# Kernel tuning notes

Measured on AMD Instinct MI355X. Metric: run time of the kernel, lower is better.

## Reference

```python
import jax, jax.numpy as jnp
import numpy as np

B, L, E, H, W = 2, 8192, 1024, 16, 128
HD = E // H  # 64


def setup_inputs() -> dict:
    key = jax.random.key(0)
    ks = jax.random.split(key, 9)
    s = 1.0 / np.sqrt(E)
    inp = {"x": jax.random.normal(ks[0], (B, L, E), jnp.float32)}
    for i, n in enumerate(["Wq", "Wk", "Wv", "Wo"]):
        inp[n] = jax.random.uniform(ks[1 + i], (E, E), jnp.float32, -s, s)
    for i, n in enumerate(["bq", "bk", "bv", "bo"]):
        inp[n] = jax.random.uniform(ks[5 + i], (E,), jnp.float32, -s, s)
    return inp


def _skew_prob(p, w):
    # (..., w, 2w+1) -> (..., w, 3w) with row i right-shifted by i:
    # out[..., i, i+j] = p[..., i, j]  (zeros elsewhere)
    lead = p.shape[:-2]
    M, Lc = p.shape[-2], p.shape[-1]
    p = jnp.pad(p, [(0, 0)] * len(lead) + [(0, 0), (0, M + 1)])
    p = p.reshape(*lead, M * (Lc + M + 1))[..., :-M].reshape(*lead, M, M + Lc)
    return p[..., :-1]


def _sliding_attend(q, k, v, w):
    # q,k,v: (b,h,l,d); banded attention, window w on each side (2w+1 diagonals)
    b, h, l, d = q.shape
    c = l // w
    qc = q.reshape(b, h, c, w, d)
    # per-chunk key/value windows of 3w tokens (w halo each side, zero padded)
    idx = jnp.arange(c)[:, None] * w + jnp.arange(3 * w)[None, :]  # (c, 3w)
    kw = jnp.pad(k, ((0, 0), (0, 0), (w, w), (0, 0)))[:, :, idx]  # (b,h,c,3w,d)
    s = jnp.einsum('bhcqd,bhckd->bhcqk', qc, kw)  # (b,h,c,w,3w)
    # extract band: band[i, j] = s[i, i+j], j in [0, 2w] (offset d = j - w)
    gidx = (jnp.arange(w)[:, None] + jnp.arange(2 * w + 1)[None, :])[None, None, None]
    band = jnp.take_along_axis(s, gidx, axis=-1).reshape(b, h, l, 2 * w + 1)
    # mask out-of-range positions (matches the module's edge -inf loop)
    pos = jnp.arange(l)[:, None] + (jnp.arange(2 * w + 1) - w)[None, :]
    band = jnp.where((pos >= 0) & (pos < l), band, -jnp.inf)
    prob = jax.nn.softmax(band / np.sqrt(d), axis=-1)  # scale by sqrt(head_dim)
    vw = jnp.pad(v, ((0, 0), (0, 0), (w, w), (0, 0)))[:, :, idx]  # (b,h,c,3w,d)
    p3 = _skew_prob(prob.reshape(b, h, c, w, 2 * w + 1), w)  # (b,h,c,w,3w)
    ctx = jnp.einsum('bhcqk,bhckd->bhcqd', p3, vw)
    return ctx.reshape(b, h, l, d)


def reference(x, Wq, Wk, Wv, Wo, bq, bk, bv, bo):
    q = (x @ Wq.T + bq).reshape(B, L, H, HD).transpose(0, 2, 1, 3)
    k = (x @ Wk.T + bk).reshape(B, L, H, HD).transpose(0, 2, 1, 3)
    v = (x @ Wv.T + bv).reshape(B, L, H, HD).transpose(0, 2, 1, 3)
    ctx = _sliding_attend(q, k, v, W)
    ctx = ctx.transpose(0, 2, 1, 3).reshape(B, L, E)
    return ctx @ Wo.T + bo
```

## Files before the change

### kernel.cpp

```cpp
#include <hip/hip_runtime.h>
#include <math.h>

#define B_SZ  2
#define L_SEQ 8192
#define EMB   1024
#define NH    16
#define HDIM  64
#define WIN   128
#define MROWS (B_SZ*L_SEQ)

typedef __attribute__((ext_vector_type(8))) _Float16 f16x8;
typedef __attribute__((ext_vector_type(4))) _Float16 f16x4;
typedef __attribute__((ext_vector_type(4))) float f32x4;

__device__ __forceinline__ void gload16(const void* g, void* l) {
    __builtin_amdgcn_global_load_lds(
        (const __attribute__((address_space(1))) unsigned int*)g,
        (__attribute__((address_space(3))) unsigned int*)l, 16, 0, 0);
}

__global__ __launch_bounds__(256)
void round_all(const float* __restrict__ x,
               const float* __restrict__ wq, const float* __restrict__ wk,
               const float* __restrict__ wv, const float* __restrict__ wo,
               _Float16* __restrict__ xf, _Float16* __restrict__ q16,
               _Float16* __restrict__ k16, _Float16* __restrict__ v16,
               _Float16* __restrict__ o16)
{
    const size_t NX = (size_t)MROWS * EMB, NW = (size_t)EMB * EMB;
    size_t gid = ((size_t)blockIdx.x * 256 + threadIdx.x) * 4;
    const float* src; _Float16* dst; size_t off;
    if (gid < NX)               { src = x;  dst = xf;  off = gid; }
    else if (gid < NX + NW)     { src = wq; dst = q16; off = gid - NX; }
    else if (gid < NX + 2*NW)   { src = wk; dst = k16; off = gid - NX - 2*NW + NW; }
    else if (gid < NX + 3*NW)   { src = wv; dst = v16; off = gid - NX - 2*NW; }
    else                        { src = wo; dst = o16; off = gid - NX - 3*NW; }
    float4 v = *(const float4*)(src + off);
    f16x4 o;
    o[0] = (_Float16)v.x; o[1] = (_Float16)v.y;
    o[2] = (_Float16)v.z; o[3] = (_Float16)v.w;
    *(f16x4*)(dst + off) = o;
}

__global__ __launch_bounds__(256)
void gemm_qkv(const _Float16* __restrict__ X,
              const _Float16* __restrict__ Wq, const _Float16* __restrict__ Wk,
              const _Float16* __restrict__ Wv,
              const float* __restrict__ bq, const float* __restrict__ bk,
              const float* __restrict__ bv,
              _Float16* __restrict__ qf, _Float16* __restrict__ kf,
              _Float16* __restrict__ vtf)
{
    constexpr int K = EMB;
    __shared__ char smem[34816];
    _Float16* As = (_Float16*)smem;
    _Float16* Bs = (_Float16*)(smem + 16384);

    const int id = blockIdx.x;
    const int row = (id / 192) * 8 + (id & 7);
    const int colq = (id >> 3) % 24;
    const int wsel = colq >> 3;
    const int bm = row * 128, bn = (colq & 7) * 128;
    const _Float16* Bw = wsel == 0 ? Wq : wsel == 1 ? Wk : Wv;
    const float* bias = wsel == 0 ? bq : wsel == 1 ? bk : bv;
    const float scale = wsel == 0 ? 0.125f : 1.0f;

    const int t = threadIdx.x;
    const int wave = t >> 6, lane = t & 63;
    const int srow = t >> 3;
    const int gq8 = ((t & 7) ^ (srow & 7)) * 8;
    size_t gA[4], gB[4];
    #pragma unroll
    for (int s = 0; s < 4; s++) {
        int r = s * 32 + srow;
        gA[s] = (size_t)(bm + r) * K + gq8;
        gB[s] = (size_t)(bn + r) * K + gq8;
    }
    const int lbw = wave * 1024;

    const int wr = wave >> 1, wc = wave & 1;
    const int frow = lane & 15, quad = lane >> 4;
    int aoff[4][2], boff[4][2];
    #pragma unroll
    for (int i = 0; i < 4; i++)
        #pragma unroll
        for (int ks = 0; ks < 2; ks++) {
            int slot = ((ks * 4 + quad) ^ (frow & 7)) * 16;
            aoff[i][ks] = (wr * 64 + i * 16 + frow) * 128 + slot;
            boff[i][ks] = (wc * 64 + i * 16 + frow) * 128 + slot;
        }

    f32x4 acc[4][4] = {};
    for (int k0 = 0; k0 < K; k0 += 64) {
        #pragma unroll
        for (int s = 0; s < 4; s++) {
            gload16(X  + gA[s] + k0, (char*)As + s * 4096 + lbw);
            gload16(Bw + gB[s] + k0, (char*)Bs + s * 4096 + lbw);
        }
        __syncthreads();
        #pragma unroll
        for (int ks = 0; ks < 2; ks++) {
            f16x8 af[4], bf[4];
            #pragma unroll
            for (int i = 0; i < 4; i++) {
                af[i] = *(const f16x8*)((const char*)As + aoff[i][ks]);
                bf[i] = *(const f16x8*)((const char*)Bs + boff[i][ks]);
            }
            #pragma unroll
            for (int i = 0; i < 4; i++)
                #pragma unroll
                for (int j = 0; j < 4; j++)
                    acc[i][j] = __builtin_amdgcn_mfma_f32_16x16x32_f16(af[i], bf[j], acc[i][j], 0, 0, 0);
        }
        __syncthreads();
    }

    _Float16* Ct = (_Float16*)smem;
    const int ccol = lane & 15;
    if (wsel < 2) {
        #pragma unroll
        for (int i = 0; i < 4; i++)
            #pragma unroll
            for (int j = 0; j < 4; j++) {
                int nl = wc * 64 + j * 16 + ccol;
                float bvv = bias[bn + nl];
                #pragma unroll
                for (int r = 0; r < 4; r++) {
                    int ml = wr * 64 + i * 16 + quad * 4 + r;
                    Ct[ml * 136 + nl] = (_Float16)((acc[i][j][r] + bvv) * scale);
                }
            }
        __syncthreads();
        _Float16* dst = wsel == 0 ? qf : kf;
        #pragma unroll
        for (int pass = 0; pass < 8; pass++) {
            int chunk = pass * 256 + t;
            int ml = chunk >> 4, seg = chunk & 15;
            uint4 v = *(const uint4*)&Ct[ml * 136 + seg * 8];
            int m = bm + ml, bb = m >> 13, l = m & (L_SEQ - 1);
            int n = bn + seg * 8, h = n >> 6, d = n & 63;
            *(uint4*)&dst[((size_t)(bb * NH + h) * L_SEQ + l) * HDIM + d] = v;
        }
    } else {
        #pragma unroll
        for (int i = 0; i < 4; i++)
            #pragma unroll
            for (int j = 0; j < 4; j++) {
                int nl = wc * 64 + j * 16 + ccol;
                float bvv = bias[bn + nl];
                #pragma unroll
                for (int r = 0; r < 4; r++) {
                    int ml = wr * 64 + i * 16 + quad * 4 + r;
                    Ct[nl * 136 + ml] = (_Float16)(acc[i][j][r] + bvv);
                }
            }
        __syncthreads();
        #pragma unroll
        for (int pass = 0; pass < 8; pass++) {
            int chunk = pass * 256 + t;
            int nl = chunk >> 4, seg = chunk & 15;
            uint4 v = *(const uint4*)&Ct[nl * 136 + seg * 8];
            int n = bn + nl, h = n >> 6, d = n & 63;
            int bb = bm >> 13, l = (bm & (L_SEQ - 1)) + seg * 8;
            *(uint4*)&vtf[((size_t)(bb * NH + h) * HDIM + d) * L_SEQ + l] = v;
        }
    }
}

__global__ __launch_bounds__(256)
void gemm_out(const _Float16* __restrict__ A, const _Float16* __restrict__ Bw,
              const float* __restrict__ bias, float* __restrict__ C)
{
    constexpr int K = EMB, N = EMB;
    __shared__ char smem[32768];
    _Float16* As = (_Float16*)smem;
    _Float16* Bs = (_Float16*)(smem + 16384);

    const int id = blockIdx.x;
    const int row = (id / 64) * 8 + (id & 7);
    const int bm = row * 128, bn = ((id >> 3) & 7) * 128;

    const int t = threadIdx.x;
    const int wave = t >> 6, lane = t & 63;
    const int srow = t >> 3;
    const int gq8 = ((t & 7) ^ (srow & 7)) * 8;
    size_t gA[4], gB[4];
    #pragma unroll
    for (int s = 0; s < 4; s++) {
        int r = s * 32 + srow;
        gA[s] = (size_t)(bm + r) * K + gq8;
        gB[s] = (size_t)(bn + r) * K + gq8;
    }
    const int lbw = wave * 1024;

    const int wr = wave >> 1, wc = wave & 1;
    const int frow = lane & 15, quad = lane >> 4;
    int aoff[4][2], boff[4][2];
    #pragma unroll
    for (int i = 0; i < 4; i++)
        #pragma unroll
        for (int ks = 0; ks < 2; ks++) {
            int slot = ((ks * 4 + quad) ^ (frow & 7)) * 16;
            aoff[i][ks] = (wr * 64 + i * 16 + frow) * 128 + slot;
            boff[i][ks] = (wc * 64 + i * 16 + frow) * 128 + slot;
        }

    f32x4 acc[4][4] = {};
    for (int k0 = 0; k0 < K; k0 += 64) {
        #pragma unroll
        for (int s = 0; s < 4; s++) {
            gload16(A  + gA[s] + k0, (char*)As + s * 4096 + lbw);
            gload16(Bw + gB[s] + k0, (char*)Bs + s * 4096 + lbw);
        }
        __syncthreads();
        #pragma unroll
        for (int ks = 0; ks < 2; ks++) {
            f16x8 af[4], bf[4];
            #pragma unroll
            for (int i = 0; i < 4; i++) {
                af[i] = *(const f16x8*)((const char*)As + aoff[i][ks]);
                bf[i] = *(const f16x8*)((const char*)Bs + boff[i][ks]);
            }
            #pragma unroll
            for (int i = 0; i < 4; i++)
                #pragma unroll
                for (int j = 0; j < 4; j++)
                    acc[i][j] = __builtin_amdgcn_mfma_f32_16x16x32_f16(af[i], bf[j], acc[i][j], 0, 0, 0);
        }
        __syncthreads();
    }

    const int ccol = lane & 15;
    #pragma unroll
    for (int i = 0; i < 4; i++) {
        int m0 = bm + wr * 64 + i * 16 + quad * 4;
        #pragma unroll
        for (int j = 0; j < 4; j++) {
            int n = bn + wc * 64 + j * 16 + ccol;
            float bvv = bias[n];
            #pragma unroll
            for (int r = 0; r < 4; r++)
                C[(size_t)(m0 + r) * N + n] = acc[i][j][r] + bvv;
        }
    }
}

__global__ __launch_bounds__(256)
void attn_mfma(const _Float16* __restrict__ qf, const _Float16* __restrict__ kf,
               const _Float16* __restrict__ vtf, _Float16* __restrict__ cf)
{
    __shared__ _Float16 Kf[4096], Vf[4096];
    __shared__ _Float16 Ps[4][16 * 72];

    const int t = threadIdx.x;
    const int wave = t >> 6, lane = t & 63;
    const int col = lane & 15, quad = lane >> 4;
    const int bh = blockIdx.y;
    const int q0 = blockIdx.x * 128;

    f16x8 qfr[2][2];
    #pragma unroll
    for (int g = 0; g < 2; g++) {
        size_t qidx = ((size_t)bh * L_SEQ + q0 + g * 64 + wave * 16 + col) * HDIM + quad * 8;
        qfr[g][0] = *(const f16x8*)(qf + qidx);
        qfr[g][1] = *(const f16x8*)(qf + qidx + 32);
    }

    f32x4 o[2][4] = {};
    float mrun[2][4], lrun[2][4];
    #pragma unroll
    for (int g = 0; g < 2; g++)
        #pragma unroll
        for (int r = 0; r < 4; r++) { mrun[g][r] = -3e38f; lrun[g][r] = 0.0f; }

    const int srow = t >> 3, sc = t & 7;
    _Float16* Pw = Ps[wave];

    for (int kt = 0; kt < 6; kt++) {
        const int p0 = q0 - WIN + kt * 64;
        if (p0 < 0 || p0 >= L_SEQ) continue;
        #pragma unroll
        for (int sw = 0; sw < 2; sw++) {
            int row = sw * 32 + srow;
            int gq = sc ^ (row & 7);
            size_t kgi = ((size_t)bh * L_SEQ + p0 + row) * HDIM + gq * 8;
            size_t vgi = ((size_t)bh * HDIM + row) * L_SEQ + p0 + gq * 8;
            int lb = sw * 4096 + wave * 1024;
            gload16(kf + kgi, (char*)Kf + lb);
            gload16(vtf + vgi, (char*)Vf + lb);
        }
        __syncthreads();

        #pragma unroll
        for (int g = 0; g < 2; g++) {
            f32x4 s[4] = {};
            #pragma unroll
            for (int ks = 0; ks < 2; ks++)
                #pragma unroll
                for (int n = 0; n < 4; n++) {
                    int off = (n * 16 + col) * 128 + (((ks * 4 + quad) ^ (col & 7)) * 16);
                    f16x8 kfr = *(const f16x8*)((const char*)Kf + off);
                    s[n] = __builtin_amdgcn_mfma_f32_16x16x32_f16(qfr[g][ks], kfr, s[n], 0, 0, 0);
                }
            const int rowb = q0 + g * 64 + wave * 16 + quad * 4;
            #pragma unroll
            for (int n = 0; n < 4; n++)
                #pragma unroll
                for (int r = 0; r < 4; r++) {
                    int dlt = (p0 + n * 16 + col) - (rowb + r);
                    if (dlt < -WIN || dlt > WIN) s[n][r] = -3e38f;
                }
            float mx[4];
            #pragma unroll
            for (int r = 0; r < 4; r++)
                mx[r] = fmaxf(fmaxf(s[0][r], s[1][r]), fmaxf(s[2][r], s[3][r]));
            #pragma unroll
            for (int x = 1; x < 16; x <<= 1)
                #pragma unroll
                for (int r = 0; r < 4; r++)
                    mx[r] = fmaxf(mx[r], __shfl_xor(mx[r], x, 64));
            float alpha[4];
            #pragma unroll
            for (int r = 0; r < 4; r++) {
                float mn = fmaxf(mrun[g][r], mx[r]);
                alpha[r] = __expf(mrun[g][r] - mn);
                mrun[g][r] = mn;
            }
            float sm[4] = {0.f, 0.f, 0.f, 0.f};
            #pragma unroll
            for (int n = 0; n < 4; n++)
                #pragma unroll
                for (int r = 0; r < 4; r++) {
                    float pv = __expf(s[n][r] - mrun[g][r]);
                    sm[r] += pv;
                    Pw[(quad * 4 + r) * 72 + n * 16 + col] = (_Float16)pv;
                }
            #pragma unroll
            for (int x = 1; x < 16; x <<= 1)
                #pragma unroll
                for (int r = 0; r < 4; r++)
                    sm[r] += __shfl_xor(sm[r], x, 64);
            #pragma unroll
            for (int r = 0; r < 4; r++)
                lrun[g][r] = lrun[g][r] * alpha[r] + sm[r];
            #pragma unroll
            for (int n = 0; n < 4; n++)
                #pragma unroll
                for (int r = 0; r < 4; r++)
                    o[g][n][r] *= alpha[r];
            #pragma unroll
            for (int ks = 0; ks < 2; ks++) {
                f16x8 pfr = *(const f16x8*)&Pw[col * 72 + ks * 32 + quad * 8];
                #pragma unroll
                for (int n = 0; n < 4; n++) {
                    int off = (n * 16 + col) * 128 + (((ks * 4 + quad) ^ (col & 7)) * 16);
                    f16x8 vfr = *(const f16x8*)((const char*)Vf + off);
                    o[g][n] = __builtin_amdgcn_mfma_f32_16x16x32_f16(pfr, vfr, o[g][n], 0, 0, 0);
                }
            }
        }
        __syncthreads();
    }

    const int b = bh >> 4, h = bh & 15;
    #pragma unroll
    for (int g = 0; g < 2; g++)
        #pragma unroll
        for (int r = 0; r < 4; r++) {
            float inv = 1.0f / lrun[g][r];
            int q = q0 + g * 64 + wave * 16 + quad * 4 + r;
            size_t base = ((size_t)b * L_SEQ + q) * EMB + h * HDIM;
            #pragma unroll
            for (int n = 0; n < 4; n++)
                cf[base + n * 16 + col] = (_Float16)(o[g][n][r] * inv);
        }
}

extern "C" void kernel_launch(void* const* d_in, const int* in_sizes, int n_in,
                              void* d_out, int out_size, void* d_ws, size_t ws_size,
                              hipStream_t stream) {
    const float* x  = (const float*)d_in[0];
    const float* Wq = (const float*)d_in[1];
    const float* Wk = (const float*)d_in[2];
    const float* Wv = (const float*)d_in[3];
    const float* Wo = (const float*)d_in[4];
    const float* bq = (const float*)d_in[5];
    const float* bk = (const float*)d_in[6];
    const float* bv = (const float*)d_in[7];
    const float* bo = (const float*)d_in[8];
    float* out = (float*)d_out;

    const size_t per = (size_t)B_SZ * NH * L_SEQ * HDIM;
    _Float16* w16 = (_Float16*)d_ws;
    _Float16* xf   = w16;
    _Float16* qf   = w16 + per;
    _Float16* kf   = w16 + 2 * per;
    _Float16* vtf  = w16 + 3 * per;
    _Float16* cf   = w16 + 4 * per;
    _Float16* wq16 = w16 + 5 * per;
    _Float16* wk16 = wq16 + 1048576;
    _Float16* wv16 = wq16 + 2 * 1048576;
    _Float16* wo16 = wq16 + 3 * 1048576;

    dim3 blk(256);
    const int nround = (MROWS * EMB + 4 * EMB * EMB) / 1024;
    round_all<<<nround, blk, 0, stream>>>(x, Wq, Wk, Wv, Wo, xf, wq16, wk16, wv16, wo16);

    gemm_qkv<<<3072, blk, 0, stream>>>(xf, wq16, wk16, wv16, bq, bk, bv, qf, kf, vtf);

    attn_mfma<<<dim3(L_SEQ / 128, B_SZ * NH), blk, 0, stream>>>(qf, kf, vtf, cf);

    gemm_out<<<1024, blk, 0, stream>>>(cf, wo16, bo, out);
}
```

Measured before the change: 386.4 us.

## Use 256x256 double-buffered 512-thread tiles for QKV and output GEMMs

Both projection GEMMs move from 128x128 tiles with 256 threads to 256x256 tiles with 512 threads (8 waves, each computing 128x64) and a K step of 32. A two-stage LDS ring is filled by global_load_lds, with explicit vmcnt waits and barriers so the next tile's loads overlap the current MFMAs, and s_setprio is raised around the MFMA bursts. The QKV epilogue now stages through per-wave swizzled LDS before the coalesced stores to q, k and transposed v. This aims for more data reuse per loaded byte and better latency hiding, at the cost of 64KB of LDS per block, more registers and fewer blocks in the grid.

Result: no change. 381.4 us (-1.3%).

```diff
diff --git a/kernel.cpp b/kernel.cpp
--- a/kernel.cpp
+++ b/kernel.cpp
@@ -42,7 +42,82 @@
     *(f16x4*)(dst + off) = o;
 }
 
-__global__ __launch_bounds__(256)
+
+#define QKV_LOOP_PROLOGUE(Aptr, Bptr)                                          \
+    const int t = threadIdx.x;                                                 \
+    const int wave = t >> 6, lane = t & 63;                                    \
+    const int wr = wave >> 2, wc = wave & 3;                                   \
+    const int frow = lane & 15, quad = lane >> 4;                              \
+    const int srow = t >> 2;                                                   \
+    const int schunk = (t & 3) ^ ((t >> 3) & 3);                               \
+    size_t gA[2], gB[2];                                                       \
+    _Pragma("unroll")                                                          \
+    for (int s = 0; s < 2; ++s) {                                              \
+        int r = s * 128 + srow;                                                \
+        gA[s] = (size_t)(bm + r) * 1024 + schunk * 8;                          \
+        gB[s] = (size_t)(bn + r) * 1024 + schunk * 8;                          \
+    }                                                                          \
+    const int ldst = t * 16;                                                   \
+    const int sw = (quad ^ ((frow >> 1) & 3)) * 16;                            \
+    int aoff[8], boff[4];                                                      \
+    _Pragma("unroll")                                                          \
+    for (int i = 0; i < 8; ++i) aoff[i] = (wr * 128 + i * 16 + frow) * 64 + sw;\
+    _Pragma("unroll")                                                          \
+    for (int j = 0; j < 4; ++j)                                                \
+        boff[j] = 32768 + (wc * 64 + j * 16 + frow) * 64 + sw;                 \
+    f32x4 acc[8][4] = {};                                                      \
+    _Pragma("unroll")                                                          \
+    for (int pt = 0; pt < 2; ++pt)                                             \
+        _Pragma("unroll")                                                      \
+        for (int s = 0; s < 2; ++s) {                                          \
+            gload16(Aptr + gA[s] + pt * 32, smem + pt * 16384 + s * 8192 + ldst);          \
+            gload16(Bptr + gB[s] + pt * 32, smem + 32768 + pt * 16384 + s * 8192 + ldst);  \
+        }                                                                      \
+    for (int kt = 0; kt < 32; ++kt) {                                          \
+        const int cur = kt & 1;                                                \
+        if (kt < 31) asm volatile("s_waitcnt vmcnt(4)");                       \
+        else         asm volatile("s_waitcnt vmcnt(0)");                       \
+        __builtin_amdgcn_s_barrier();                                          \
+        asm volatile("" ::: "memory");                                         \
+        const char* Ab = (const char*)smem + cur * 16384;                      \
+        f16x8 af[4], bf[4];                                                    \
+        _Pragma("unroll")                                                      \
+        for (int j = 0; j < 4; ++j) bf[j] = *(const f16x8*)(Ab + boff[j] * 2 - boff[j] + boff[j]); \
+        _Pragma("unroll")                                                      \
+        for (int j = 0; j < 4; ++j) bf[j] = *(const f16x8*)(Ab + boff[j]);     \
+        _Pragma("unroll")                                                      \
+        for (int i = 0; i < 4; ++i) af[i] = *(const f16x8*)(Ab + aoff[i] * 1); \
+        __builtin_amdgcn_s_setprio(1);                                         \
+        _Pragma("unroll")                                                      \
+        for (int i = 0; i < 4; ++i)                                            \
+            _Pragma("unroll")                                                  \
+            for (int j = 0; j < 4; ++j)                                        \
+                acc[i][j] = __builtin_amdgcn_mfma_f32_16x16x32_f16(af[i], bf[j], acc[i][j], 0, 0, 0); \
+        __builtin_amdgcn_s_setprio(0);                                         \
+        _Pragma("unroll")                                                      \
+        for (int i = 0; i < 4; ++i) af[i] = *(const f16x8*)(Ab + aoff[i + 4]); \
+        __builtin_amdgcn_s_setprio(1);                                         \
+        _Pragma("unroll")                                                      \
+        for (int i = 0; i < 4; ++i)                                            \
+            _Pragma("unroll")                                                  \
+            for (int j = 0; j < 4; ++j)                                        \
+                acc[i + 4][j] = __builtin_amdgcn_mfma_f32_16x16x32_f16(af[i], bf[j], acc[i + 4][j], 0, 0, 0); \
+        __builtin_amdgcn_s_setprio(0);                                         \
+        asm volatile("" ::: "memory");                                         \
+        __builtin_amdgcn_s_barrier();                                          \
+        asm volatile("" ::: "memory");                                         \
+        if (kt + 2 < 32) {                                                     \
+            const int ko = (kt + 2) * 32;                                      \
+            _Pragma("unroll")                                                  \
+            for (int s = 0; s < 2; ++s) {                                      \
+                gload16(Aptr + gA[s] + ko, smem + cur * 16384 + s * 8192 + ldst);          \
+                gload16(Bptr + gB[s] + ko, smem + 32768 + cur * 16384 + s * 8192 + ldst);  \
+            }                                                                  \
+        }                                                                      \
+    }
+
+
+__global__ __launch_bounds__(512, 2)
 void gemm_qkv(const _Float16* __restrict__ X,
               const _Float16* __restrict__ Wq, const _Float16* __restrict__ Wk,
               const _Float16* __restrict__ Wv,
@@ -51,195 +126,105 @@
               _Float16* __restrict__ qf, _Float16* __restrict__ kf,
               _Float16* __restrict__ vtf)
 {
-    constexpr int K = EMB;
-    __shared__ char smem[34816];
-    _Float16* As = (_Float16*)smem;
-    _Float16* Bs = (_Float16*)(smem + 16384);
+    __shared__ __attribute__((aligned(16))) char smem[65536];
 
     const int id = blockIdx.x;
-    const int row = (id / 192) * 8 + (id & 7);
-    const int colq = (id >> 3) % 24;
-    const int wsel = colq >> 3;
-    const int bm = row * 128, bn = (colq & 7) * 128;
+    const int row = (id / 96) * 8 + (id & 7);
+    const int colq = (id >> 3) % 12;
+    const int wsel = colq >> 2;
+    const int bm = row * 256, bn = (colq & 3) * 256;
     const _Float16* Bw = wsel == 0 ? Wq : wsel == 1 ? Wk : Wv;
     const float* bias = wsel == 0 ? bq : wsel == 1 ? bk : bv;
     const float scale = wsel == 0 ? 0.125f : 1.0f;
 
-    const int t = threadIdx.x;
-    const int wave = t >> 6, lane = t & 63;
-    const int srow = t >> 3;
-    const int gq8 = ((t & 7) ^ (srow & 7)) * 8;
-    size_t gA[4], gB[4];
-    #pragma unroll
-    for (int s = 0; s < 4; s++) {
-        int r = s * 32 + srow;
-        gA[s] = (size_t)(bm + r) * K + gq8;
-        gB[s] = (size_t)(bn + r) * K + gq8;
-    }
-    const int lbw = wave * 1024;
-
-    const int wr = wave >> 1, wc = wave & 1;
-    const int frow = lane & 15, quad = lane >> 4;
-    int aoff[4][2], boff[4][2];
-    #pragma unroll
-    for (int i = 0; i < 4; i++)
-        #pragma unroll
-        for (int ks = 0; ks < 2; ks++) {
-            int slot = ((ks * 4 + quad) ^ (frow & 7)) * 16;
-            aoff[i][ks] = (wr * 64 + i * 16 + frow) * 128 + slot;
-            boff[i][ks] = (wc * 64 + i * 16 + frow) * 128 + slot;
-        }
-
-    f32x4 acc[4][4] = {};
-    for (int k0 = 0; k0 < K; k0 += 64) {
-        #pragma unroll
-        for (int s = 0; s < 4; s++) {
-            gload16(X  + gA[s] + k0, (char*)As + s * 4096 + lbw);
-            gload16(Bw + gB[s] + k0, (char*)Bs + s * 4096 + lbw);
-        }
-        __syncthreads();
-        #pragma unroll
-        for (int ks = 0; ks < 2; ks++) {
-            f16x8 af[4], bf[4];
-            #pragma unroll
-            for (int i = 0; i < 4; i++) {
-                af[i] = *(const f16x8*)((const char*)As + aoff[i][ks]);
-                bf[i] = *(const f16x8*)((const char*)Bs + boff[i][ks]);
+    QKV_LOOP_PROLOGUE(X, Bw)
+
+    char* Cw = smem + wave * 8192;
+    const int bb = bm >> 13;
+    const int l0 = (bm & (L_SEQ - 1)) + wr * 128;
+    const int h = (bn >> 6) + wc;
+    if (wsel < 2) {
+        _Float16* dst = wsel == 0 ? qf : kf;
+        const size_t hb = ((size_t)(bb * NH + h)) * L_SEQ * HDIM;
+        #pragma unroll
+        for (int ih = 0; ih < 2; ++ih) {
+            asm volatile("" ::: "memory");
+            #pragma unroll
+            for (int i = 0; i < 4; ++i)
+                #pragma unroll
+                for (int j = 0; j < 4; ++j) {
+                    const int lc = j * 16 + frow;
+                    const float bvv = bias[bn + wc * 64 + lc];
+                    #pragma unroll
+                    for (int r = 0; r < 4; ++r) {
+                        const int lr = i * 16 + quad * 4 + r;
+                        const int bo = lr * 128 + ((lc * 2) ^ ((lr & 7) << 4));
+                        *(_Float16*)(Cw + bo) = (_Float16)((acc[ih * 4 + i][j][r] + bvv) * scale);
+                    }
+                }
+            asm volatile("" ::: "memory");
+            #pragma unroll
+            for (int p = 0; p < 8; ++p) {
+                const int idx = p * 64 + lane;
+                const int lr = idx >> 3, seg = idx & 7;
+                const int bo = lr * 128 + ((seg * 16) ^ ((lr & 7) << 4));
+                uint4 v = *(const uint4*)(Cw + bo);
+                *(uint4*)&dst[hb + (size_t)(l0 + ih * 64 + lr) * HDIM + seg * 8] = v;
             }
-            #pragma unroll
-            for (int i = 0; i < 4; i++)
-                #pragma unroll
-                for (int j = 0; j < 4; j++)
-                    acc[i][j] = __builtin_amdgcn_mfma_f32_16x16x32_f16(af[i], bf[j], acc[i][j], 0, 0, 0);
-        }
-        __syncthreads();
-    }
-
-    _Float16* Ct = (_Float16*)smem;
-    const int ccol = lane & 15;
-    if (wsel < 2) {
-        #pragma unroll
-        for (int i = 0; i < 4; i++)
-            #pragma unroll
-            for (int j = 0; j < 4; j++) {
-                int nl = wc * 64 + j * 16 + ccol;
-                float bvv = bias[bn + nl];
-                #pragma unroll
-                for (int r = 0; r < 4; r++) {
-                    int ml = wr * 64 + i * 16 + quad * 4 + r;
-                    Ct[ml * 136 + nl] = (_Float16)((acc[i][j][r] + bvv) * scale);
-                }
+        }
+    } else {
+        const size_t hb = ((size_t)(bb * NH + h)) * HDIM * L_SEQ;
+        #pragma unroll
+        for (int ih = 0; ih < 2; ++ih) {
+            asm volatile("" ::: "memory");
+            #pragma unroll
+            for (int i = 0; i < 4; ++i)
+                #pragma unroll
+                for (int j = 0; j < 4; ++j) {
+                    const int lc = j * 16 + frow;
+                    const float bvv = bias[bn + wc * 64 + lc];
+                    #pragma unroll
+                    for (int r = 0; r < 4; ++r) {
+                        const int lr = i * 16 + quad * 4 + r;
+                        const int bo = lc * 128 + ((lr * 2) ^ ((lc & 7) << 4));
+                        *(_Float16*)(Cw + bo) = (_Float16)(acc[ih * 4 + i][j][r] + bvv);
+                    }
+                }
+            asm volatile("" ::: "memory");
+            #pragma unroll
+            for (int p = 0; p < 8; ++p) {
+                const int idx = p * 64 + lane;
+                const int dc = idx >> 3, sl = idx & 7;
+                const int bo = dc * 128 + ((sl * 16) ^ ((dc & 7) << 4));
+                uint4 v = *(const uint4*)(Cw + bo);
+                *(uint4*)&vtf[hb + (size_t)dc * L_SEQ + (l0 + ih * 64 + sl * 8)] = v;
             }
-        __syncthreads();
-        _Float16* dst = wsel == 0 ? qf : kf;
-        #pragma unroll
-        for (int pass = 0; pass < 8; pass++) {
-            int chunk = pass * 256 + t;
-            int ml = chunk >> 4, seg = chunk & 15;
-            uint4 v = *(const uint4*)&Ct[ml * 136 + seg * 8];
-            int m = bm + ml, bb = m >> 13, l = m & (L_SEQ - 1);
-            int n = bn + seg * 8, h = n >> 6, d = n & 63;
-            *(uint4*)&dst[((size_t)(bb * NH + h) * L_SEQ + l) * HDIM + d] = v;
-        }
-    } else {
-        #pragma unroll
-        for (int i = 0; i < 4; i++)
-            #pragma unroll
-            for (int j = 0; j < 4; j++) {
-                int nl = wc * 64 + j * 16 + ccol;
-                float bvv = bias[bn + nl];
-                #pragma unroll
-                for (int r = 0; r < 4; r++) {
-                    int ml = wr * 64 + i * 16 + quad * 4 + r;
-                    Ct[nl * 136 + ml] = (_Float16)(acc[i][j][r] + bvv);
-                }
-            }
-        __syncthreads();
-        #pragma unroll
-        for (int pass = 0; pass < 8; pass++) {
-            int chunk = pass * 256 + t;
-            int nl = chunk >> 4, seg = chunk & 15;
-            uint4 v = *(const uint4*)&Ct[nl * 136 + seg * 8];
-            int n = bn + nl, h = n >> 6, d = n & 63;
-            int bb = bm >> 13, l = (bm & (L_SEQ - 1)) + seg * 8;
-            *(uint4*)&vtf[((size_t)(bb * NH + h) * HDIM + d) * L_SEQ + l] = v;
-        }
-    }
-}
-
-__global__ __launch_bounds__(256)
-void gemm_out(const _Float16* __restrict__ A, const _Float16* __restrict__ Bw,
+        }
+    }
+}
+
+__global__ __launch_bounds__(512, 2)
+void gemm_out(const _Float16* __restrict__ A, const _Float16* __restrict__ Bwm,
               const float* __restrict__ bias, float* __restrict__ C)
 {
-    constexpr int K = EMB, N = EMB;
-    __shared__ char smem[32768];
-    _Float16* As = (_Float16*)smem;
-    _Float16* Bs = (_Float16*)(smem + 16384);
+    constexpr int N = EMB;
+    __shared__ __attribute__((aligned(16))) char smem[65536];
 
     const int id = blockIdx.x;
-    const int row = (id / 64) * 8 + (id & 7);
-    const int bm = row * 128, bn = ((id >> 3) & 7) * 128;
-
-    const int t = threadIdx.x;
-    const int wave = t >> 6, lane = t & 63;
-    const int srow = t >> 3;
-    const int gq8 = ((t & 7) ^ (srow & 7)) * 8;
-    size_t gA[4], gB[4];
+    const int row = (id / 32) * 8 + (id & 7);
+    const int bm = row * 256, bn = ((id >> 3) & 3) * 256;
+
+    QKV_LOOP_PROLOGUE(A, Bwm)
+
     #pragma unroll
-    for (int s = 0; s < 4; s++) {
-        int r = s * 32 + srow;
-        gA[s] = (size_t)(bm + r) * K + gq8;
-        gB[s] = (size_t)(bn + r) * K + gq8;
-    }
-    const int lbw = wave * 1024;
-
-    const int wr = wave >> 1, wc = wave & 1;
-    const int frow = lane & 15, quad = lane >> 4;
-    int aoff[4][2], boff[4][2];
-    #pragma unroll
-    for (int i = 0; i < 4; i++)
-        #pragma unroll
-        for (int ks = 0; ks < 2; ks++) {
-            int slot = ((ks * 4 + quad) ^ (frow & 7)) * 16;
-            aoff[i][ks] = (wr * 64 + i * 16 + frow) * 128 + slot;
-            boff[i][ks] = (wc * 64 + i * 16 + frow) * 128 + slot;
-        }
-
-    f32x4 acc[4][4] = {};
-    for (int k0 = 0; k0 < K; k0 += 64) {
-        #pragma unroll
-        for (int s = 0; s < 4; s++) {
-            gload16(A  + gA[s] + k0, (char*)As + s * 4096 + lbw);
-            gload16(Bw + gB[s] + k0, (char*)Bs + s * 4096 + lbw);
-        }
-        __syncthreads();
-        #pragma unroll
-        for (int ks = 0; ks < 2; ks++) {
-            f16x8 af[4], bf[4];
-            #pragma unroll
-            for (int i = 0; i < 4; i++) {
-                af[i] = *(const f16x8*)((const char*)As + aoff[i][ks]);
-                bf[i] = *(const f16x8*)((const char*)Bs + boff[i][ks]);
-            }
-            #pragma unroll
-            for (int i = 0; i < 4; i++)
-                #pragma unroll
-                for (int j = 0; j < 4; j++)
-                    acc[i][j] = __builtin_amdgcn_mfma_f32_16x16x32_f16(af[i], bf[j], acc[i][j], 0, 0, 0);
-        }
-        __syncthreads();
-    }
-
-    const int ccol = lane & 15;
-    #pragma unroll
-    for (int i = 0; i < 4; i++) {
-        int m0 = bm + wr * 64 + i * 16 + quad * 4;
-        #pragma unroll
-        for (int j = 0; j < 4; j++) {
-            int n = bn + wc * 64 + j * 16 + ccol;
+    for (int i = 0; i < 8; ++i) {
+        int m0 = bm + wr * 128 + i * 16 + quad * 4;
+        #pragma unroll
+        for (int j = 0; j < 4; ++j) {
+            int n = bn + wc * 64 + j * 16 + frow;
             float bvv = bias[n];
             #pragma unroll
-            for (int r = 0; r < 4; r++)
+            for (int r = 0; r < 4; ++r)
                 C[(size_t)(m0 + r) * N + n] = acc[i][j][r] + bvv;
         }
     }
@@ -280,12 +265,12 @@
         const int p0 = q0 - WIN + kt * 64;
         if (p0 < 0 || p0 >= L_SEQ) continue;
         #pragma unroll
-        for (int sw = 0; sw < 2; sw++) {
-            int row = sw * 32 + srow;
+        for (int sw2 = 0; sw2 < 2; sw2++) {
+            int row = sw2 * 32 + srow;
             int gq = sc ^ (row & 7);
             size_t kgi = ((size_t)bh * L_SEQ + p0 + row) * HDIM + gq * 8;
             size_t vgi = ((size_t)bh * HDIM + row) * L_SEQ + p0 + gq * 8;
-            int lb = sw * 4096 + wave * 1024;
+            int lb = sw2 * 4096 + wave * 1024;
             gload16(kf + kgi, (char*)Kf + lb);
             gload16(vtf + vgi, (char*)Vf + lb);
         }
@@ -402,13 +387,12 @@
     _Float16* wv16 = wq16 + 2 * 1048576;
     _Float16* wo16 = wq16 + 3 * 1048576;
 
-    dim3 blk(256);
     const int nround = (MROWS * EMB + 4 * EMB * EMB) / 1024;
-    round_all<<<nround, blk, 0, stream>>>(x, Wq, Wk, Wv, Wo, xf, wq16, wk16, wv16, wo16);
-
-    gemm_qkv<<<3072, blk, 0, stream>>>(xf, wq16, wk16, wv16, bq, bk, bv, qf, kf, vtf);
-
-    attn_mfma<<<dim3(L_SEQ / 128, B_SZ * NH), blk, 0, stream>>>(qf, kf, vtf, cf);
-
-    gemm_out<<<1024, blk, 0, stream>>>(cf, wo16, bo, out);
-}
+    round_all<<<nround, dim3(256), 0, stream>>>(x, Wq, Wk, Wv, Wo, xf, wq16, wk16, wv16, wo16);
+
+    gemm_qkv<<<768, dim3(512), 0, stream>>>(xf, wq16, wk16, wv16, bq, bk, bv, qf, kf, vtf);
+
+    attn_mfma<<<dim3(L_SEQ / 128, B_SZ * NH), dim3(256), 0, stream>>>(qf, kf, vtf, cf);
+
+    gemm_out<<<256, dim3(512), 0, stream>>>(cf, wo16, bo, out);
+}
```
